# Kernel optimization log

Hardware: AMD Instinct MI355X
Metric: run time of the kernel (lower is better)

The kernel has to match this reference:

```python
import jax, jax.numpy as jnp
import numpy as np

B, S, D, H, DFF = 4, 2048, 1024, 16, 4096
DK = D // H


def layer_norm(x, g, b, eps=1e-5):
    mu = jnp.mean(x, axis=-1, keepdims=True)
    var = jnp.mean((x - mu) ** 2, axis=-1, keepdims=True)
    return (x - mu) / jnp.sqrt(var + eps) * g + b


def setup_inputs() -> dict:
    key = jax.random.key(0)
    ks = jax.random.split(key, 16)
    w = lambda k, shape: jax.random.normal(k, shape, jnp.float32) * 0.02
    return {
        "x": jax.random.normal(ks[0], (B, S, D), jnp.float32),
        "w_q": w(ks[1], (D, D)), "b_q": jnp.zeros((D,), jnp.float32),
        "w_k": w(ks[2], (D, D)), "b_k": jnp.zeros((D,), jnp.float32),
        "w_v": w(ks[3], (D, D)), "b_v": jnp.zeros((D,), jnp.float32),
        "w_o": w(ks[4], (D, D)), "b_o": jnp.zeros((D,), jnp.float32),
        "w_g": w(ks[5], (D, H)), "b_g": jnp.zeros((H,), jnp.float32),
        "w1": w(ks[6], (D, DFF)), "b1": jnp.zeros((DFF,), jnp.float32),
        "w2": w(ks[7], (DFF, D)), "b2": jnp.zeros((D,), jnp.float32),
        "g1": jnp.ones((D,), jnp.float32), "beta1": jnp.zeros((D,), jnp.float32),
        "g2": jnp.ones((D,), jnp.float32), "beta2": jnp.zeros((D,), jnp.float32),
        "mask": jnp.ones((B, 1, 1, S), jnp.int32),
    }


def reference(x, w_q, b_q, w_k, b_k, w_v, b_v, w_o, b_o, w_g, b_g,
              w1, b1, w2, b2, g1, beta1, g2, beta2, mask):
    b, s, d = x.shape
    scale = DK ** -0.5
    # QKV projections -> [B,H,S,DK]
    q = (x @ w_q + b_q).reshape(b, s, H, DK).transpose(0, 2, 1, 3)
    k = (x @ w_k + b_k).reshape(b, s, H, DK).transpose(0, 2, 1, 3)
    v = (x @ w_v + b_v).reshape(b, s, H, DK).transpose(0, 2, 1, 3)
    scores = jnp.einsum("bhqd,bhkd->bhqk", q, k) * scale  # [B,H,S,S]
    scores = jnp.where(mask == 0, jnp.float32(-1e9), scores)
    attn = jax.nn.softmax(scores, axis=-1)
    # per-(token, head) sigmoid gate applied post-softmax
    gate = jax.nn.sigmoid(x @ w_g + b_g)            # [B,S,H]
    attn = attn * gate.transpose(0, 2, 1)[..., None]  # [B,H,S,1]
    ctx = jnp.einsum("bhqk,bhkd->bhqd", attn, v)
    ctx = ctx.transpose(0, 2, 1, 3).reshape(b, s, d)
    attn_out = ctx @ w_o + b_o
    x1 = layer_norm(x + attn_out, g1, beta1)
    ff = jax.nn.gelu(x1 @ w1 + b1, approximate=False) @ w2 + b2
    return layer_norm(x1 + ff, g2, beta2)
```

## Files before the change

### kernel.cpp

```cpp
#include <hip/hip_runtime.h>
#include <hip/hip_bf16.h>
#include <cstdint>


typedef __bf16 bf16x8 __attribute__((ext_vector_type(8)));
typedef float  f32x4  __attribute__((ext_vector_type(4)));

__device__ __forceinline__ uint16_t f2bf_bits(float f) {
    __hip_bfloat16 h = __float2bfloat16(f);
    return __builtin_bit_cast(uint16_t, h);
}

#define GLOAD16(ldsb, gp) __builtin_amdgcn_global_load_lds( \
    (const __attribute__((address_space(1))) void*)(gp),    \
    (__attribute__((address_space(3))) void*)(ldsb), 16, 0, 0)

__global__ __launch_bounds__(256) void cast_bf16_kernel(
    const float* __restrict__ in, __hip_bfloat16* __restrict__ out, size_t n4)
{
    size_t i = (size_t)blockIdx.x * blockDim.x + threadIdx.x;
    if (i >= n4) return;
    float4 v = ((const float4*)in)[i];
    ushort4 o;
    o.x = f2bf_bits(v.x); o.y = f2bf_bits(v.y);
    o.z = f2bf_bits(v.z); o.w = f2bf_bits(v.w);
    ((ushort4*)out)[i] = o;
}

__global__ __launch_bounds__(256) void transpose_cast_kernel(
    const float* __restrict__ in, __hip_bfloat16* __restrict__ out, int K, int N)
{
    __shared__ float t[32][33];
    int n0 = blockIdx.x * 32, k0 = blockIdx.y * 32;
    int tx = threadIdx.x, ty = threadIdx.y;
#pragma unroll
    for (int i = 0; i < 4; ++i)
        t[ty + i * 8][tx] = in[(size_t)(k0 + ty + i * 8) * N + n0 + tx];
    __syncthreads();
#pragma unroll
    for (int i = 0; i < 4; ++i)
        out[(size_t)(n0 + ty + i * 8) * K + k0 + tx] = __float2bfloat16(t[tx][ty + i * 8]);
}

__global__ __launch_bounds__(256) void gate_kernel(
    const float* __restrict__ x, const float* __restrict__ wg,
    const float* __restrict__ bg, float* __restrict__ gate)
{
    int tid = threadIdx.x, lane = tid & 63, wid = tid >> 6;
    int row = blockIdx.x * 4 + wid;
    const float* xr = x + (size_t)row * 1024;
    float acc[16];
#pragma unroll
    for (int hh = 0; hh < 16; ++hh) acc[hh] = 0.0f;
    for (int k = lane; k < 1024; k += 64) {
        float xv = xr[k];
        const float* wr = wg + (size_t)k * 16;
#pragma unroll
        for (int hh = 0; hh < 16; ++hh) acc[hh] = fmaf(xv, wr[hh], acc[hh]);
    }
#pragma unroll
    for (int hh = 0; hh < 16; ++hh) {
#pragma unroll
        for (int d = 1; d < 64; d <<= 1) acc[hh] += __shfl_xor(acc[hh], d);
    }
    if (lane < 16) {
        float v = 0.0f;
#pragma unroll
        for (int hh = 0; hh < 16; ++hh)
            if (lane == hh) v = acc[hh] + bg[hh];
        gate[(size_t)row * 16 + lane] = 1.0f / (1.0f + __expf(-v));
    }
}

__global__ __launch_bounds__(256) void ln_kernel(
    const float* __restrict__ A, const float* __restrict__ Bx,
    const float* __restrict__ g, const float* __restrict__ beta,
    float* __restrict__ outf, __hip_bfloat16* __restrict__ outb)
{
    int row = blockIdx.x, tid = threadIdx.x;
    const float4* a4 = (const float4*)(A  + (size_t)row * 1024);
    const float4* b4 = (const float4*)(Bx + (size_t)row * 1024);
    float4 va = a4[tid], vb = b4[tid];
    float x0 = va.x + vb.x, x1 = va.y + vb.y, x2 = va.z + vb.z, x3 = va.w + vb.w;
    float s  = x0 + x1 + x2 + x3;
    float sq = x0 * x0 + x1 * x1 + x2 * x2 + x3 * x3;
#pragma unroll
    for (int d = 1; d < 64; d <<= 1) { s += __shfl_xor(s, d); sq += __shfl_xor(sq, d); }
    __shared__ float ss[4], ssq[4];
    int wid = tid >> 6, lane = tid & 63;
    if (lane == 0) { ss[wid] = s; ssq[wid] = sq; }
    __syncthreads();
    s  = ss[0] + ss[1] + ss[2] + ss[3];
    sq = ssq[0] + ssq[1] + ssq[2] + ssq[3];
    float mean = s * (1.0f / 1024.0f);
    float var  = sq * (1.0f / 1024.0f) - mean * mean;
    float rstd = rsqrtf(var + 1e-5f);
    float4 gv = ((const float4*)g)[tid], bv = ((const float4*)beta)[tid];
    float y0 = (x0 - mean) * rstd * gv.x + bv.x;
    float y1 = (x1 - mean) * rstd * gv.y + bv.y;
    float y2 = (x2 - mean) * rstd * gv.z + bv.z;
    float y3 = (x3 - mean) * rstd * gv.w + bv.w;
    float4 o; o.x = y0; o.y = y1; o.z = y2; o.w = y3;
    ((float4*)(outf + (size_t)row * 1024))[tid] = o;
    if (outb) {
        ushort4 ob;
        ob.x = f2bf_bits(y0); ob.y = f2bf_bits(y1);
        ob.z = f2bf_bits(y2); ob.w = f2bf_bits(y3);
        ((ushort4*)(outb + (size_t)row * 1024))[tid] = ob;
    }
}

template<int EPI>
__global__ __launch_bounds__(256, 2) void gemm128(
    const __hip_bfloat16* __restrict__ A,
    const __hip_bfloat16* __restrict__ BT,
    const float* __restrict__ bias,
    void* __restrict__ Cout, int M, int N, int K)
{
    __shared__ __align__(16) __hip_bfloat16 As[128 * 64];
    __shared__ __align__(16) __hip_bfloat16 Bs[128 * 64];
    const int tid = threadIdx.x, lane = tid & 63, wid = tid >> 6;
    const int bx = blockIdx.x, by = blockIdx.y;
    const int wr = wid >> 1, wc = wid & 1;

    f32x4 acc[4][4];
#pragma unroll
    for (int i = 0; i < 4; ++i)
#pragma unroll
        for (int j = 0; j < 4; ++j) acc[i][j] = (f32x4){0.f, 0.f, 0.f, 0.f};

    const char* Abase = (const char*)A  + (size_t)(by * 128) * K * 2;
    const char* Bbase = (const char*)BT + (size_t)(bx * 128) * K * 2;
    char* AsB = (char*)As; char* BsB = (char*)Bs;
    const int laneRow = lane >> 3;
    const int laneCol = (lane & 7) * 16;

    for (int ks = 0; ks < K; ks += 64) {
#pragma unroll
        for (int j = 0; j < 4; ++j) {
            int r = j * 32 + wid * 8 + laneRow;
            size_t goff = (size_t)r * K * 2 + (size_t)ks * 2 + laneCol;
            GLOAD16(AsB + j * 4096 + wid * 1024, Abase + goff);
            GLOAD16(BsB + j * 4096 + wid * 1024, Bbase + goff);
        }
        __syncthreads();
#pragma unroll
        for (int kk = 0; kk < 2; ++kk) {
            const int kob = (kk * 32 + (lane >> 4) * 8) * 2;
            bf16x8 a[4], b[4];
#pragma unroll
            for (int mt = 0; mt < 4; ++mt)
                a[mt] = *(const bf16x8*)(AsB + (wr * 64 + mt * 16 + (lane & 15)) * 128 + kob);
#pragma unroll
            for (int nt = 0; nt < 4; ++nt)
                b[nt] = *(const bf16x8*)(BsB + (wc * 64 + nt * 16 + (lane & 15)) * 128 + kob);
#pragma unroll
            for (int mt = 0; mt < 4; ++mt)
#pragma unroll
                for (int nt = 0; nt < 4; ++nt)
                    acc[mt][nt] = __builtin_amdgcn_mfma_f32_16x16x32_bf16(
                        a[mt], b[nt], acc[mt][nt], 0, 0, 0);
        }
        __syncthreads();
    }

    const int m0 = by * 128 + wr * 64;
    const int n0 = bx * 128 + wc * 64;
#pragma unroll
    for (int mt = 0; mt < 4; ++mt) {
#pragma unroll
        for (int nt = 0; nt < 4; ++nt) {
            int n = n0 + nt * 16 + (lane & 15);
            float bv = bias[n];
#pragma unroll
            for (int j = 0; j < 4; ++j) {
                int m = m0 + mt * 16 + (lane >> 4) * 4 + j;
                float v = acc[mt][nt][j] + bv;
                if constexpr (EPI == 0) {
                    ((float*)Cout)[(size_t)m * N + n] = v;
                } else if constexpr (EPI == 1) {
                    int b = m >> 11, s = m & 2047, h = n >> 6, dk = n & 63;
                    ((__hip_bfloat16*)Cout)[((((size_t)b * 16 + h) * 2048 + s) << 6) + dk] =
                        __float2bfloat16(v * 0.125f);
                } else if constexpr (EPI == 2) {
                    int b = m >> 11, s = m & 2047, h = n >> 6, dk = n & 63;
                    ((__hip_bfloat16*)Cout)[((((size_t)b * 16 + h) * 2048 + s) << 6) + dk] =
                        __float2bfloat16(v);
                } else if constexpr (EPI == 3) {
                    int b = m >> 11, s = m & 2047, h = n >> 6, dk = n & 63;
                    ((__hip_bfloat16*)Cout)[(((size_t)b * 16 + h) * 64 + dk) * 2048 + s] =
                        __float2bfloat16(v);
                } else if constexpr (EPI == 4) {
                    float ge = 0.5f * v * (1.0f + erff(v * 0.70710678118654752f));
                    ((__hip_bfloat16*)Cout)[(size_t)m * N + n] = __float2bfloat16(ge);
                }
            }
        }
    }
}

__global__ __launch_bounds__(256, 2) void attn_kernel(
    const __hip_bfloat16* __restrict__ Q,
    const __hip_bfloat16* __restrict__ Kg,
    const __hip_bfloat16* __restrict__ Vt,
    const float* __restrict__ gate,
    const int* __restrict__ mask,
    __hip_bfloat16* __restrict__ ctx)
{
    __shared__ __align__(16) __hip_bfloat16 Ks[64 * 64];
    __shared__ __align__(16) __hip_bfloat16 Vs[64 * 64];
    __shared__ __align__(16) __hip_bfloat16 Ps[4][16 * 64];
    const int tid = threadIdx.x, lane = tid & 63, wid = tid >> 6;
    const int qt = blockIdx.x, bh = blockIdx.y;
    const int b = bh >> 4, h = bh & 15;
    const int q0 = qt * 64 + wid * 16;

    bf16x8 aq[2];
    const __hip_bfloat16* Qbase = Q + ((size_t)bh * 2048 + q0) * 64;
#pragma unroll
    for (int kk = 0; kk < 2; ++kk)
        aq[kk] = *(const bf16x8*)(Qbase + (lane & 15) * 64 + kk * 32 + (lane >> 4) * 8);

    f32x4 octx[4];
#pragma unroll
    for (int dt = 0; dt < 4; ++dt) octx[dt] = (f32x4){0.f, 0.f, 0.f, 0.f};
    float m_run[4], l_run[4];
#pragma unroll
    for (int r = 0; r < 4; ++r) { m_run[r] = -1e30f; l_run[r] = 0.0f; }

    const char* Kbase = (const char*)(Kg + (size_t)bh * 2048 * 64);
    const char* Vbase = (const char*)(Vt + (size_t)bh * 64 * 2048);
    char* KsB = (char*)Ks; char* VsB = (char*)Vs;
    char* PsB = (char*)&Ps[wid][0];
    const int laneRow = lane >> 3, laneColB = (lane & 7) * 16;

    for (int kv0 = 0; kv0 < 2048; kv0 += 64) {
#pragma unroll
        for (int j = 0; j < 2; ++j) {
            int off = j * 4096 + wid * 1024;
            GLOAD16(KsB + off, Kbase + (size_t)kv0 * 128 + off + lane * 16);
            int dk = j * 32 + wid * 8 + laneRow;
            GLOAD16(VsB + off, Vbase + (size_t)dk * 4096 + (size_t)kv0 * 2 + laneColB);
        }
        __syncthreads();

        f32x4 sfr[4];
#pragma unroll
        for (int ct = 0; ct < 4; ++ct) sfr[ct] = (f32x4){0.f, 0.f, 0.f, 0.f};
#pragma unroll
        for (int kk = 0; kk < 2; ++kk) {
            const int kob = (kk * 32 + (lane >> 4) * 8) * 2;
#pragma unroll
            for (int ct = 0; ct < 4; ++ct) {
                bf16x8 bk = *(const bf16x8*)(KsB + (ct * 16 + (lane & 15)) * 128 + kob);
                sfr[ct] = __builtin_amdgcn_mfma_f32_16x16x32_bf16(aq[kk], bk, sfr[ct], 0, 0, 0);
            }
        }
#pragma unroll
        for (int ct = 0; ct < 4; ++ct) {
            int kvi = kv0 + ct * 16 + (lane & 15);
            if (mask[b * 2048 + kvi] == 0) {
                sfr[ct][0] = -1e9f; sfr[ct][1] = -1e9f;
                sfr[ct][2] = -1e9f; sfr[ct][3] = -1e9f;
            }
        }
#pragma unroll
        for (int r = 0; r < 4; ++r) {
            float mx = fmaxf(fmaxf(sfr[0][r], sfr[1][r]), fmaxf(sfr[2][r], sfr[3][r]));
            mx = fmaxf(mx, __shfl_xor(mx, 1));
            mx = fmaxf(mx, __shfl_xor(mx, 2));
            mx = fmaxf(mx, __shfl_xor(mx, 4));
            mx = fmaxf(mx, __shfl_xor(mx, 8));
            float mn = fmaxf(m_run[r], mx);
            float c  = __expf(m_run[r] - mn);
            m_run[r] = mn;
            float s = 0.0f;
#pragma unroll
            for (int ct = 0; ct < 4; ++ct) {
                float p = __expf(sfr[ct][r] - mn);
                sfr[ct][r] = p;
                s += p;
            }
            s += __shfl_xor(s, 1); s += __shfl_xor(s, 2);
            s += __shfl_xor(s, 4); s += __shfl_xor(s, 8);
            l_run[r] = l_run[r] * c + s;
#pragma unroll
            for (int dt = 0; dt < 4; ++dt) octx[dt][r] *= c;
        }
#pragma unroll
        for (int ct = 0; ct < 4; ++ct) {
#pragma unroll
            for (int r = 0; r < 4; ++r) {
                int qr = (lane >> 4) * 4 + r;
                int byteoff = (qr * 128 + (ct * 16 + (lane & 15)) * 2) ^ ((qr & 7) << 4);
                *(__hip_bfloat16*)(PsB + byteoff) = __float2bfloat16(sfr[ct][r]);
            }
        }
#pragma unroll
        for (int kk = 0; kk < 2; ++kk) {
            const int kb = kk * 32 + (lane >> 4) * 8;
            int pbyte = ((lane & 15) * 128 + kb * 2) ^ (((lane & 15) & 7) << 4);
            bf16x8 ap = *(const bf16x8*)(PsB + pbyte);
#pragma unroll
            for (int dt = 0; dt < 4; ++dt) {
                bf16x8 bvv = *(const bf16x8*)(VsB + (dt * 16 + (lane & 15)) * 128 + kb * 2);
                octx[dt] = __builtin_amdgcn_mfma_f32_16x16x32_bf16(ap, bvv, octx[dt], 0, 0, 0);
            }
        }
        __syncthreads();
    }

#pragma unroll
    for (int r = 0; r < 4; ++r) {
        int qg = q0 + (lane >> 4) * 4 + r;
        size_t rowm = (size_t)b * 2048 + qg;
        float gv = gate[rowm * 16 + h];
        float inv = gv / l_run[r];
#pragma unroll
        for (int dt = 0; dt < 4; ++dt)
            ctx[rowm * 1024 + h * 64 + dt * 16 + (lane & 15)] =
                __float2bfloat16(octx[dt][r] * inv);
    }
}

extern "C" void kernel_launch(void* const* d_in, const int* in_sizes, int n_in,
                              void* d_out, int out_size, void* d_ws, size_t ws_size,
                              hipStream_t stream)
{
    const float* x    = (const float*)d_in[0];
    const float* w_q  = (const float*)d_in[1];
    const float* b_q  = (const float*)d_in[2];
    const float* w_k  = (const float*)d_in[3];
    const float* b_k  = (const float*)d_in[4];
    const float* w_v  = (const float*)d_in[5];
    const float* b_v  = (const float*)d_in[6];
    const float* w_o  = (const float*)d_in[7];
    const float* b_o  = (const float*)d_in[8];
    const float* w_g  = (const float*)d_in[9];
    const float* b_g  = (const float*)d_in[10];
    const float* w1   = (const float*)d_in[11];
    const float* b1   = (const float*)d_in[12];
    const float* w2   = (const float*)d_in[13];
    const float* b2   = (const float*)d_in[14];
    const float* g1   = (const float*)d_in[15];
    const float* be1  = (const float*)d_in[16];
    const float* g2   = (const float*)d_in[17];
    const float* be2  = (const float*)d_in[18];
    const int*   mask = (const int*)d_in[19];

    char* ws = (char*)d_ws;
    size_t off = 0;
    auto alloc = [&](size_t bytes) -> char* {
        char* p = ws + off; off += (bytes + 255) & ~(size_t)255; return p;
    };

    char* regionA = alloc(67108864);
    __hip_bfloat16* xb   = (__hip_bfloat16*)regionA;
    __hip_bfloat16* qb   = (__hip_bfloat16*)(regionA + 16777216);
    __hip_bfloat16* kb   = (__hip_bfloat16*)(regionA + 33554432);
    __hip_bfloat16* vb   = (__hip_bfloat16*)(regionA + 50331648);
    __hip_bfloat16* hbuf = (__hip_bfloat16*)regionA;

    __hip_bfloat16* wqT = (__hip_bfloat16*)alloc(2097152);
    __hip_bfloat16* wkT = (__hip_bfloat16*)alloc(2097152);
    __hip_bfloat16* wvT = (__hip_bfloat16*)alloc(2097152);
    __hip_bfloat16* woT = (__hip_bfloat16*)alloc(2097152);
    __hip_bfloat16* w1T = (__hip_bfloat16*)alloc(8388608);
    __hip_bfloat16* w2T = (__hip_bfloat16*)alloc(8388608);
    float* gate       = (float*)alloc(524288);
    __hip_bfloat16* ctx = (__hip_bfloat16*)alloc(16777216);
    float* attn_out   = (float*)alloc(33554432);
    float* x1f        = (float*)alloc(33554432);
    __hip_bfloat16* x1b = (__hip_bfloat16*)alloc(16777216);

    dim3 tb(32, 8);
    cast_bf16_kernel<<<8192, 256, 0, stream>>>(x, xb, 2097152);
    transpose_cast_kernel<<<dim3(32, 32),  tb, 0, stream>>>(w_q, wqT, 1024, 1024);
    transpose_cast_kernel<<<dim3(32, 32),  tb, 0, stream>>>(w_k, wkT, 1024, 1024);
    transpose_cast_kernel<<<dim3(32, 32),  tb, 0, stream>>>(w_v, wvT, 1024, 1024);
    transpose_cast_kernel<<<dim3(32, 32),  tb, 0, stream>>>(w_o, woT, 1024, 1024);
    transpose_cast_kernel<<<dim3(128, 32), tb, 0, stream>>>(w1, w1T, 1024, 4096);
    transpose_cast_kernel<<<dim3(32, 128), tb, 0, stream>>>(w2, w2T, 4096, 1024);
    gate_kernel<<<2048, 256, 0, stream>>>(x, w_g, b_g, gate);

    dim3 g1024(8, 64);
    gemm128<1><<<g1024, 256, 0, stream>>>(xb, wqT, b_q, qb, 8192, 1024, 1024);
    gemm128<2><<<g1024, 256, 0, stream>>>(xb, wkT, b_k, kb, 8192, 1024, 1024);
    gemm128<3><<<g1024, 256, 0, stream>>>(xb, wvT, b_v, vb, 8192, 1024, 1024);

    attn_kernel<<<dim3(32, 64), 256, 0, stream>>>(qb, kb, vb, gate, mask, ctx);

    gemm128<0><<<g1024, 256, 0, stream>>>(ctx, woT, b_o, attn_out, 8192, 1024, 1024);
    ln_kernel<<<8192, 256, 0, stream>>>(x, attn_out, g1, be1, x1f, x1b);
    gemm128<4><<<dim3(32, 64), 256, 0, stream>>>(x1b, w1T, b1, hbuf, 8192, 4096, 1024);
    gemm128<0><<<g1024, 256, 0, stream>>>(hbuf, w2T, b2, attn_out, 8192, 1024, 4096);
    ln_kernel<<<8192, 256, 0, stream>>>(x1f, attn_out, g2, be2, (float*)d_out, nullptr);
}
```

Measured before the change: 799.3 us.

## Add pipelined 256x256 GEMM, fuse QKV projections, swizzle attention LDS

Adds a 512-thread GEMM kernel with 256x256 tiles, double-buffered LDS staging through global_load_lds, an XOR swizzle, priority hints and a chiplet-aware block remap. It is used for a single fused QKV projection (N=3072, with a per-region epilogue) and for the GELU FFN1 GEMM. The attention kernel gets a linearised, XCD-interleaved block order and XOR-swizzled K/V LDS layouts to cut bank conflicts. The fused QKV relies on wqT, wkT and wvT being contiguous in memory, and the larger tiles raise register and LDS pressure.

```diff
diff --git a/kernel.cpp b/kernel.cpp
--- a/kernel.cpp
+++ b/kernel.cpp
@@ -176,23 +176,161 @@
             for (int j = 0; j < 4; ++j) {
                 int m = m0 + mt * 16 + (lane >> 4) * 4 + j;
                 float v = acc[mt][nt][j] + bv;
-                if constexpr (EPI == 0) {
-                    ((float*)Cout)[(size_t)m * N + n] = v;
-                } else if constexpr (EPI == 1) {
-                    int b = m >> 11, s = m & 2047, h = n >> 6, dk = n & 63;
-                    ((__hip_bfloat16*)Cout)[((((size_t)b * 16 + h) * 2048 + s) << 6) + dk] =
-                        __float2bfloat16(v * 0.125f);
-                } else if constexpr (EPI == 2) {
-                    int b = m >> 11, s = m & 2047, h = n >> 6, dk = n & 63;
-                    ((__hip_bfloat16*)Cout)[((((size_t)b * 16 + h) * 2048 + s) << 6) + dk] =
-                        __float2bfloat16(v);
-                } else if constexpr (EPI == 3) {
-                    int b = m >> 11, s = m & 2047, h = n >> 6, dk = n & 63;
-                    ((__hip_bfloat16*)Cout)[(((size_t)b * 16 + h) * 64 + dk) * 2048 + s] =
-                        __float2bfloat16(v);
-                } else if constexpr (EPI == 4) {
-                    float ge = 0.5f * v * (1.0f + erff(v * 0.70710678118654752f));
-                    ((__hip_bfloat16*)Cout)[(size_t)m * N + n] = __float2bfloat16(ge);
+                ((float*)Cout)[(size_t)m * N + n] = v;
+            }
+        }
+    }
+}
+
+template<int EPI>
+__global__ __launch_bounds__(512, 2) void gemm256(
+    const __hip_bfloat16* __restrict__ A,
+    const __hip_bfloat16* __restrict__ BT,
+    const float* __restrict__ bias0,
+    const float* __restrict__ bias1,
+    const float* __restrict__ bias2,
+    __hip_bfloat16* __restrict__ out0,
+    __hip_bfloat16* __restrict__ out1,
+    __hip_bfloat16* __restrict__ out2,
+    int M, int N, int K)
+{
+    __shared__ __align__(16) char lds_[131072];
+    const int tid = threadIdx.x;
+    const int lane = tid & 63;
+    const int l15 = lane & 15;
+    const int wid = tid >> 6;
+    const int wm = wid >> 2, wn = wid & 3;
+
+    const int NBX = N >> 8;
+    const int cpx = ((M >> 8) * NBX) >> 3;
+    const int nl = ((int)blockIdx.x & 7) * cpx + ((int)blockIdx.x >> 3);
+    const int by = nl / NBX, bx = nl % NBX;
+
+    const char* Abase = (const char*)A  + (size_t)(by * 256) * K * 2;
+    const char* Bbase = (const char*)BT + (size_t)(bx * 256) * K * 2;
+
+    const int srow = tid >> 3;
+    const int ssw  = ((tid & 7) ^ (srow & 7)) * 16;
+
+    f32x4 acc[8][4];
+#pragma unroll
+    for (int i = 0; i < 8; ++i)
+#pragma unroll
+        for (int j = 0; j < 4; ++j) acc[i][j] = (f32x4){0.f, 0.f, 0.f, 0.f};
+
+    auto stageA = [&](int d, int c, int ks) {
+        const char* src = Abase + ((size_t)(c * 64 + srow) * K + ks) * 2 + ssw;
+        GLOAD16(lds_ + d * 65536 + c * 8192 + wid * 1024, src);
+    };
+    auto stageB = [&](int d, int c, int ks) {
+        const char* src = Bbase + ((size_t)(c * 64 + srow) * K + ks) * 2 + ssw;
+        GLOAD16(lds_ + d * 65536 + 32768 + c * 8192 + wid * 1024, src);
+    };
+
+    const int NT = K >> 6;
+    stageB(0, 0, 0); stageB(0, 1, 0); stageB(0, 2, 0); stageB(0, 3, 0);
+    stageA(0, 0, 0); stageA(0, 2, 0); stageA(0, 1, 0); stageA(0, 3, 0);
+    asm volatile("s_waitcnt vmcnt(0)" ::: "memory");
+    __builtin_amdgcn_s_barrier();
+
+    for (int t = 0; t < NT; ++t) {
+        const int cur = t & 1, nxt = cur ^ 1;
+        const int ksn = (t + 1) << 6;
+        const bool st = (t + 1 < NT);
+        const char* ldsA = lds_ + cur * 65536;
+        const char* ldsB = ldsA + 32768;
+
+        bf16x8 bfr[4][2];
+#pragma unroll
+        for (int p = 0; p < 4; ++p) {
+            if (p == 0) {
+#pragma unroll
+                for (int nf = 0; nf < 4; ++nf) {
+                    const int br = wn * 64 + nf * 16 + l15;
+#pragma unroll
+                    for (int kk = 0; kk < 2; ++kk) {
+                        const int kb = kk * 64 + (lane >> 4) * 16;
+                        bfr[nf][kk] = *(const bf16x8*)(ldsB + (br >> 6) * 8192 +
+                            (br & 63) * 128 + (kb ^ ((br & 7) << 4)));
+                    }
+                }
+            }
+            bf16x8 afr[2][2];
+#pragma unroll
+            for (int mi = 0; mi < 2; ++mi) {
+                const int ar = wm * 128 + (2 * p + mi) * 16 + l15;
+#pragma unroll
+                for (int kk = 0; kk < 2; ++kk) {
+                    const int kb = kk * 64 + (lane >> 4) * 16;
+                    afr[mi][kk] = *(const bf16x8*)(ldsA + (ar >> 6) * 8192 +
+                        (ar & 63) * 128 + (kb ^ ((ar & 7) << 4)));
+                }
+            }
+            if (st) {
+                if      (p == 0) { stageB(nxt, 0, ksn); stageB(nxt, 1, ksn); }
+                else if (p == 1) { stageB(nxt, 2, ksn); stageB(nxt, 3, ksn); }
+                else if (p == 2) { stageA(nxt, 0, ksn); stageA(nxt, 2, ksn); }
+                else             { stageA(nxt, 1, ksn); stageA(nxt, 3, ksn); }
+            }
+            __builtin_amdgcn_s_barrier();
+            __builtin_amdgcn_s_setprio(1);
+#pragma unroll
+            for (int mi = 0; mi < 2; ++mi)
+#pragma unroll
+                for (int nf = 0; nf < 4; ++nf)
+#pragma unroll
+                    for (int kk = 0; kk < 2; ++kk)
+                        acc[2 * p + mi][nf] = __builtin_amdgcn_mfma_f32_16x16x32_bf16(
+                            afr[mi][kk], bfr[nf][kk], acc[2 * p + mi][nf], 0, 0, 0);
+            __builtin_amdgcn_s_setprio(0);
+            if (p == 1) asm volatile("s_waitcnt vmcnt(4)" ::: "memory");
+            if (p == 3) asm volatile("s_waitcnt vmcnt(2)" ::: "memory");
+            __builtin_amdgcn_s_barrier();
+        }
+    }
+
+    const int nbase = bx * 256 + wn * 64;
+    const int mbase = by * 256 + wm * 128;
+    if constexpr (EPI == 5) {
+        const int reg = nbase >> 10;
+        const float* bias = (reg == 0) ? bias0 : (reg == 1) ? bias1 : bias2;
+#pragma unroll
+        for (int mf = 0; mf < 8; ++mf) {
+#pragma unroll
+            for (int nf = 0; nf < 4; ++nf) {
+                const int n = nbase + nf * 16 + l15;
+                const int nn = n & 1023, h = nn >> 6, dk = nn & 63;
+                const float bv = bias[nn];
+#pragma unroll
+                for (int j = 0; j < 4; ++j) {
+                    const int m = mbase + mf * 16 + (lane >> 4) * 4 + j;
+                    const int b = m >> 11, s = m & 2047;
+                    const float v = acc[mf][nf][j] + bv;
+                    if (reg == 0)
+                        out0[((((size_t)b * 16 + h) * 2048 + s) << 6) + dk] =
+                            __float2bfloat16(v * 0.125f);
+                    else if (reg == 1)
+                        out1[((((size_t)b * 16 + h) * 2048 + s) << 6) + dk] =
+                            __float2bfloat16(v);
+                    else
+                        out2[(((size_t)b * 16 + h) * 64 + dk) * 2048 + s] =
+                            __float2bfloat16(v);
+                }
+            }
+        }
+    } else {
+#pragma unroll
+        for (int mf = 0; mf < 8; ++mf) {
+#pragma unroll
+            for (int nf = 0; nf < 4; ++nf) {
+                const int n = nbase + nf * 16 + l15;
+                const float bv = bias0[n];
+#pragma unroll
+                for (int j = 0; j < 4; ++j) {
+                    const int m = mbase + mf * 16 + (lane >> 4) * 4 + j;
+                    const float v = acc[mf][nf][j] + bv;
+                    const float ge = 0.5f * v * (1.0f + erff(v * 0.70710678118654752f));
+                    out0[(size_t)m * N + n] = __float2bfloat16(ge);
                 }
             }
         }
@@ -211,7 +349,10 @@
     __shared__ __align__(16) __hip_bfloat16 Vs[64 * 64];
     __shared__ __align__(16) __hip_bfloat16 Ps[4][16 * 64];
     const int tid = threadIdx.x, lane = tid & 63, wid = tid >> 6;
-    const int qt = blockIdx.x, bh = blockIdx.y;
+
+    int lin = blockIdx.x;
+    int nl  = (lin & 7) * 256 + (lin >> 3);
+    const int bh = nl >> 5, qt = nl & 31;
     const int b = bh >> 4, h = bh & 15;
     const int q0 = qt * 64 + wid * 16;
 
@@ -232,15 +373,18 @@
     const char* Vbase = (const char*)(Vt + (size_t)bh * 64 * 2048);
     char* KsB = (char*)Ks; char* VsB = (char*)Vs;
     char* PsB = (char*)&Ps[wid][0];
-    const int laneRow = lane >> 3, laneColB = (lane & 7) * 16;
+
+    const int srow = (lane >> 3);
+    const int schunk = lane & 7;
 
     for (int kv0 = 0; kv0 < 2048; kv0 += 64) {
 #pragma unroll
         for (int j = 0; j < 2; ++j) {
             int off = j * 4096 + wid * 1024;
-            GLOAD16(KsB + off, Kbase + (size_t)kv0 * 128 + off + lane * 16);
-            int dk = j * 32 + wid * 8 + laneRow;
-            GLOAD16(VsB + off, Vbase + (size_t)dk * 4096 + (size_t)kv0 * 2 + laneColB);
+            int row = j * 32 + wid * 8 + srow;
+            int sc  = (schunk ^ (row & 7)) * 16;
+            GLOAD16(KsB + off, Kbase + (size_t)(kv0 + row) * 128 + sc);
+            GLOAD16(VsB + off, Vbase + (size_t)row * 4096 + (size_t)kv0 * 2 + sc);
         }
         __syncthreads();
 
@@ -252,7 +396,8 @@
             const int kob = (kk * 32 + (lane >> 4) * 8) * 2;
 #pragma unroll
             for (int ct = 0; ct < 4; ++ct) {
-                bf16x8 bk = *(const bf16x8*)(KsB + (ct * 16 + (lane & 15)) * 128 + kob);
+                int krow = ct * 16 + (lane & 15);
+                bf16x8 bk = *(const bf16x8*)(KsB + ((krow * 128 + kob) ^ ((krow & 7) << 4)));
                 sfr[ct] = __builtin_amdgcn_mfma_f32_16x16x32_bf16(aq[kk], bk, sfr[ct], 0, 0, 0);
             }
         }
@@ -303,7 +448,8 @@
             bf16x8 ap = *(const bf16x8*)(PsB + pbyte);
 #pragma unroll
             for (int dt = 0; dt < 4; ++dt) {
-                bf16x8 bvv = *(const bf16x8*)(VsB + (dt * 16 + (lane & 15)) * 128 + kb * 2);
+                int vrow = dt * 16 + (lane & 15);
+                bf16x8 bvv = *(const bf16x8*)(VsB + ((vrow * 128 + kb * 2) ^ ((vrow & 7) << 4)));
                 octx[dt] = __builtin_amdgcn_mfma_f32_16x16x32_bf16(ap, bvv, octx[dt], 0, 0, 0);
             }
         }
@@ -383,16 +529,15 @@
     transpose_cast_kernel<<<dim3(32, 128), tb, 0, stream>>>(w2, w2T, 4096, 1024);
     gate_kernel<<<2048, 256, 0, stream>>>(x, w_g, b_g, gate);
 
-    dim3 g1024(8, 64);
-    gemm128<1><<<g1024, 256, 0, stream>>>(xb, wqT, b_q, qb, 8192, 1024, 1024);
-    gemm128<2><<<g1024, 256, 0, stream>>>(xb, wkT, b_k, kb, 8192, 1024, 1024);
-    gemm128<3><<<g1024, 256, 0, stream>>>(xb, wvT, b_v, vb, 8192, 1024, 1024);
-
-    attn_kernel<<<dim3(32, 64), 256, 0, stream>>>(qb, kb, vb, gate, mask, ctx);
-
-    gemm128<0><<<g1024, 256, 0, stream>>>(ctx, woT, b_o, attn_out, 8192, 1024, 1024);
+    gemm256<5><<<384, 512, 0, stream>>>(xb, wqT, b_q, b_k, b_v, qb, kb, vb,
+                                        8192, 3072, 1024);
+
+    attn_kernel<<<2048, 256, 0, stream>>>(qb, kb, vb, gate, mask, ctx);
+
+    gemm128<0><<<dim3(8, 64), 256, 0, stream>>>(ctx, woT, b_o, attn_out, 8192, 1024, 1024);
     ln_kernel<<<8192, 256, 0, stream>>>(x, attn_out, g1, be1, x1f, x1b);
-    gemm128<4><<<dim3(32, 64), 256, 0, stream>>>(x1b, w1T, b1, hbuf, 8192, 4096, 1024);
-    gemm128<0><<<g1024, 256, 0, stream>>>(hbuf, w2T, b2, attn_out, 8192, 1024, 4096);
+    gemm256<6><<<512, 512, 0, stream>>>(x1b, w1T, b1, nullptr, nullptr,
+                                        hbuf, nullptr, nullptr, 8192, 4096, 1024);
+    gemm128<0><<<dim3(8, 64), 256, 0, stream>>>(hbuf, w2T, b2, attn_out, 8192, 1024, 4096);
     ln_kernel<<<8192, 256, 0, stream>>>(x1f, attn_out, g2, be2, (float*)d_out, nullptr);
 }
```

Result: faster. 776.3 us (-2.9%).

## Rework attention softmax with exp2, lazy wave-wide max rescale, and swizzled LDS

Applied to the files above, without the earlier changes.

Folds log2(e) into the Q scale so the attention kernel can use raw v_exp_f32 (exp2). It replaces the per-row online max with one wave-wide max that is updated only when a new score exceeds it by more than a threshold, and it defers the row-sum shuffles to the end. It also XOR-swizzles K/V tiles in LDS to avoid bank conflicts, hoists the mask loads before the barrier, adds s_setprio around the MFMA sections, and remaps block indices so consecutive blocks are spread across heads. The aim is to cut exp and shuffle work and LDS conflicts in the inner loop. The catch is that a wave-wide max with lazy rescale can leave rows whose own max sits far below the shared max, which risks precision loss or underflow for those rows.

```diff
diff --git a/kernel.cpp b/kernel.cpp
--- a/kernel.cpp
+++ b/kernel.cpp
@@ -11,9 +11,17 @@
     return __builtin_bit_cast(uint16_t, h);
 }
 
+__device__ __forceinline__ float fast_exp2(float x) {
+    float r;
+    asm("v_exp_f32 %0, %1" : "=v"(r) : "v"(x));
+    return r;
+}
+
 #define GLOAD16(ldsb, gp) __builtin_amdgcn_global_load_lds( \
     (const __attribute__((address_space(1))) void*)(gp),    \
     (__attribute__((address_space(3))) void*)(ldsb), 16, 0, 0)
+
+#define QSCALE_LOG2E 0.18033688011112f
 
 __global__ __launch_bounds__(256) void cast_bf16_kernel(
     const float* __restrict__ in, __hip_bfloat16* __restrict__ out, size_t n4)
@@ -181,7 +189,7 @@
                 } else if constexpr (EPI == 1) {
                     int b = m >> 11, s = m & 2047, h = n >> 6, dk = n & 63;
                     ((__hip_bfloat16*)Cout)[((((size_t)b * 16 + h) * 2048 + s) << 6) + dk] =
-                        __float2bfloat16(v * 0.125f);
+                        __float2bfloat16(v * QSCALE_LOG2E);
                 } else if constexpr (EPI == 2) {
                     int b = m >> 11, s = m & 2047, h = n >> 6, dk = n & 63;
                     ((__hip_bfloat16*)Cout)[((((size_t)b * 16 + h) * 2048 + s) << 6) + dk] =
@@ -211,7 +219,10 @@
     __shared__ __align__(16) __hip_bfloat16 Vs[64 * 64];
     __shared__ __align__(16) __hip_bfloat16 Ps[4][16 * 64];
     const int tid = threadIdx.x, lane = tid & 63, wid = tid >> 6;
-    const int qt = blockIdx.x, bh = blockIdx.y;
+
+    int lin = blockIdx.x;
+    int nl  = (lin & 7) * 256 + (lin >> 3);
+    const int bh = nl >> 5, qt = nl & 31;
     const int b = bh >> 4, h = bh & 15;
     const int q0 = qt * 64 + wid * 16;
 
@@ -224,78 +235,93 @@
     f32x4 octx[4];
 #pragma unroll
     for (int dt = 0; dt < 4; ++dt) octx[dt] = (f32x4){0.f, 0.f, 0.f, 0.f};
-    float m_run[4], l_run[4];
-#pragma unroll
-    for (int r = 0; r < 4; ++r) { m_run[r] = -1e30f; l_run[r] = 0.0f; }
+    float l_part[4] = {0.f, 0.f, 0.f, 0.f};
+    float m_cur = 0.0f;
 
     const char* Kbase = (const char*)(Kg + (size_t)bh * 2048 * 64);
     const char* Vbase = (const char*)(Vt + (size_t)bh * 64 * 2048);
     char* KsB = (char*)Ks; char* VsB = (char*)Vs;
     char* PsB = (char*)&Ps[wid][0];
-    const int laneRow = lane >> 3, laneColB = (lane & 7) * 16;
+
+    const int srow = (lane >> 3);
+    const int schunk = lane & 7;
 
     for (int kv0 = 0; kv0 < 2048; kv0 += 64) {
 #pragma unroll
         for (int j = 0; j < 2; ++j) {
             int off = j * 4096 + wid * 1024;
-            GLOAD16(KsB + off, Kbase + (size_t)kv0 * 128 + off + lane * 16);
-            int dk = j * 32 + wid * 8 + laneRow;
-            GLOAD16(VsB + off, Vbase + (size_t)dk * 4096 + (size_t)kv0 * 2 + laneColB);
+            int row = j * 32 + wid * 8 + srow;
+            int sc  = (schunk ^ (row & 7)) * 16;
+            GLOAD16(KsB + off, Kbase + (size_t)(kv0 + row) * 128 + sc);
+            GLOAD16(VsB + off, Vbase + (size_t)row * 4096 + (size_t)kv0 * 2 + sc);
+        }
+        float madd[4];
+#pragma unroll
+        for (int ct = 0; ct < 4; ++ct) {
+            int kvi = kv0 + ct * 16 + (lane & 15);
+            madd[ct] = (mask[b * 2048 + kvi] == 0) ? -1e9f : 0.0f;
         }
         __syncthreads();
 
         f32x4 sfr[4];
 #pragma unroll
         for (int ct = 0; ct < 4; ++ct) sfr[ct] = (f32x4){0.f, 0.f, 0.f, 0.f};
+        __builtin_amdgcn_s_setprio(1);
 #pragma unroll
         for (int kk = 0; kk < 2; ++kk) {
             const int kob = (kk * 32 + (lane >> 4) * 8) * 2;
 #pragma unroll
             for (int ct = 0; ct < 4; ++ct) {
-                bf16x8 bk = *(const bf16x8*)(KsB + (ct * 16 + (lane & 15)) * 128 + kob);
+                int krow = ct * 16 + (lane & 15);
+                bf16x8 bk = *(const bf16x8*)(KsB + ((krow * 128 + kob) ^ ((krow & 7) << 4)));
                 sfr[ct] = __builtin_amdgcn_mfma_f32_16x16x32_bf16(aq[kk], bk, sfr[ct], 0, 0, 0);
             }
         }
+        __builtin_amdgcn_s_setprio(0);
 #pragma unroll
         for (int ct = 0; ct < 4; ++ct) {
-            int kvi = kv0 + ct * 16 + (lane & 15);
-            if (mask[b * 2048 + kvi] == 0) {
-                sfr[ct][0] = -1e9f; sfr[ct][1] = -1e9f;
-                sfr[ct][2] = -1e9f; sfr[ct][3] = -1e9f;
-            }
-        }
-#pragma unroll
-        for (int r = 0; r < 4; ++r) {
-            float mx = fmaxf(fmaxf(sfr[0][r], sfr[1][r]), fmaxf(sfr[2][r], sfr[3][r]));
-            mx = fmaxf(mx, __shfl_xor(mx, 1));
-            mx = fmaxf(mx, __shfl_xor(mx, 2));
-            mx = fmaxf(mx, __shfl_xor(mx, 4));
-            mx = fmaxf(mx, __shfl_xor(mx, 8));
-            float mn = fmaxf(m_run[r], mx);
-            float c  = __expf(m_run[r] - mn);
-            m_run[r] = mn;
-            float s = 0.0f;
-#pragma unroll
-            for (int ct = 0; ct < 4; ++ct) {
-                float p = __expf(sfr[ct][r] - mn);
-                sfr[ct][r] = p;
-                s += p;
-            }
-            s += __shfl_xor(s, 1); s += __shfl_xor(s, 2);
-            s += __shfl_xor(s, 4); s += __shfl_xor(s, 8);
-            l_run[r] = l_run[r] * c + s;
-#pragma unroll
-            for (int dt = 0; dt < 4; ++dt) octx[dt][r] *= c;
-        }
+#pragma unroll
+            for (int r = 0; r < 4; ++r) sfr[ct][r] += madd[ct];
+        }
+
+        float mlane = sfr[0][0];
+#pragma unroll
+        for (int ct = 0; ct < 4; ++ct)
+#pragma unroll
+            for (int r = 0; r < 4; ++r) mlane = fmaxf(mlane, sfr[ct][r]);
+
+        if (kv0 == 0) {
+            float wm = mlane;
+#pragma unroll
+            for (int d = 1; d < 64; d <<= 1) wm = fmaxf(wm, __shfl_xor(wm, d));
+            m_cur = wm;
+        } else if (!__all(mlane <= m_cur + 11.0f)) {
+            float wm = mlane;
+#pragma unroll
+            for (int d = 1; d < 64; d <<= 1) wm = fmaxf(wm, __shfl_xor(wm, d));
+            wm = fmaxf(wm, m_cur);
+            float c = fast_exp2(m_cur - wm);
+            m_cur = wm;
+#pragma unroll
+            for (int dt = 0; dt < 4; ++dt)
+#pragma unroll
+                for (int r = 0; r < 4; ++r) octx[dt][r] *= c;
+#pragma unroll
+            for (int r = 0; r < 4; ++r) l_part[r] *= c;
+        }
+
 #pragma unroll
         for (int ct = 0; ct < 4; ++ct) {
 #pragma unroll
             for (int r = 0; r < 4; ++r) {
+                float p = fast_exp2(sfr[ct][r] - m_cur);
+                l_part[r] += p;
                 int qr = (lane >> 4) * 4 + r;
                 int byteoff = (qr * 128 + (ct * 16 + (lane & 15)) * 2) ^ ((qr & 7) << 4);
-                *(__hip_bfloat16*)(PsB + byteoff) = __float2bfloat16(sfr[ct][r]);
+                *(__hip_bfloat16*)(PsB + byteoff) = __float2bfloat16(p);
             }
         }
+        __builtin_amdgcn_s_setprio(1);
 #pragma unroll
         for (int kk = 0; kk < 2; ++kk) {
             const int kb = kk * 32 + (lane >> 4) * 8;
@@ -303,11 +329,21 @@
             bf16x8 ap = *(const bf16x8*)(PsB + pbyte);
 #pragma unroll
             for (int dt = 0; dt < 4; ++dt) {
-                bf16x8 bvv = *(const bf16x8*)(VsB + (dt * 16 + (lane & 15)) * 128 + kb * 2);
+                int vrow = dt * 16 + (lane & 15);
+                bf16x8 bvv = *(const bf16x8*)(VsB + ((vrow * 128 + kb * 2) ^ ((vrow & 7) << 4)));
                 octx[dt] = __builtin_amdgcn_mfma_f32_16x16x32_bf16(ap, bvv, octx[dt], 0, 0, 0);
             }
         }
+        __builtin_amdgcn_s_setprio(0);
         __syncthreads();
+    }
+
+#pragma unroll
+    for (int r = 0; r < 4; ++r) {
+        float s = l_part[r];
+        s += __shfl_xor(s, 1); s += __shfl_xor(s, 2);
+        s += __shfl_xor(s, 4); s += __shfl_xor(s, 8);
+        l_part[r] = s;
     }
 
 #pragma unroll
@@ -315,7 +351,7 @@
         int qg = q0 + (lane >> 4) * 4 + r;
         size_t rowm = (size_t)b * 2048 + qg;
         float gv = gate[rowm * 16 + h];
-        float inv = gv / l_run[r];
+        float inv = gv / l_part[r];
 #pragma unroll
         for (int dt = 0; dt < 4; ++dt)
             ctx[rowm * 1024 + h * 64 + dt * 16 + (lane & 15)] =
@@ -388,7 +424,7 @@
     gemm128<2><<<g1024, 256, 0, stream>>>(xb, wkT, b_k, kb, 8192, 1024, 1024);
     gemm128<3><<<g1024, 256, 0, stream>>>(xb, wvT, b_v, vb, 8192, 1024, 1024);
 
-    attn_kernel<<<dim3(32, 64), 256, 0, stream>>>(qb, kb, vb, gate, mask, ctx);
+    attn_kernel<<<2048, 256, 0, stream>>>(qb, kb, vb, gate, mask, ctx);
 
     gemm128<0><<<g1024, 256, 0, stream>>>(ctx, woT, b_o, attn_out, 8192, 1024, 1024);
     ln_kernel<<<8192, 256, 0, stream>>>(x, attn_out, g1, be1, x1f, x1b);
```

Result: faster. 648.8 us (-18.8%).
